# Kernel tuning notes

Hardware: AMD Instinct MI355X
Metric: run time of the kernel (lower is better)

The kernel has to match this reference:

```python
import jax, jax.numpy as jnp
import numpy as np

B, S, D = 64, 256, 768   # batch, max_seq_length, bert hidden
CAP = 8                  # semantic_cap_size (= num_capsules)
NT = 10                  # ntasks (= num_routes)
TASK = 5
NUM_ITER = 3


def squash(t, axis=-1):
    sq = jnp.sum(t * t, axis=axis, keepdims=True)
    return (sq / (1.0 + sq)) * t / jnp.sqrt(sq)


def setup_inputs() -> dict:
    key = jax.random.key(0)
    k0, k1, k2, k3 = jax.random.split(key, 4)
    x = jax.random.normal(k0, (B, S, D), dtype=jnp.float32)
    # per-task semantic projections: ntasks x Linear(768 -> CAP)
    fc1_w = jax.random.normal(k1, (NT, CAP, D), dtype=jnp.float32) * 0.02
    fc1_b = jnp.zeros((NT, CAP), dtype=jnp.float32)
    # route_weights: [num_capsules, num_routes, in_channel=S*CAP, class_dim=S]
    route_weights = jax.random.normal(k2, (CAP, NT, S * CAP, S), dtype=jnp.float32)
    # larger: Linear(CAP -> 768)
    larger_w = jax.random.normal(k3, (D, CAP), dtype=jnp.float32) * 0.02
    larger_b = jnp.zeros((D,), dtype=jnp.float32)
    return {"x": x, "task": TASK, "fc1_w": fc1_w, "fc1_b": fc1_b,
            "route_weights": route_weights, "larger_w": larger_w, "larger_b": larger_b}


def reference(x, task, fc1_w, fc1_b, route_weights, larger_w, larger_b):
    Bb, Ss, _ = x.shape
    nt, cap, _ = fc1_w.shape
    # --- semantic capsules: per-task Linear, cat over task dim, squash over tasks ---
    sem = jnp.einsum('bsd,ncd->bscn', x, fc1_w) + fc1_b.T[None, None]  # [B,S,CAP,NT]
    sem = sem.reshape(Bb, Ss * cap, nt)          # matches torch view(B,-1,1)+cat
    sem = squash(sem, axis=-1)
    u = jnp.transpose(sem, (0, 2, 1))            # [B, NT, S*CAP] (transpose(2,1))
    # --- tsv capsules: dynamic routing ---
    priors = jnp.einsum('brk,crkl->cbrl', u, route_weights)[:, :, :, None, :]  # [CAP,B,NT,1,S]
    tsv = jnp.tril(jnp.ones((nt, nt), dtype=x.dtype))
    tsv_t = tsv[task].reshape(1, 1, nt, 1, 1)
    mask = jnp.where(tsv[task] == 0, jnp.float32(-10000.0), jnp.float32(0.0)).reshape(1, 1, nt, 1, 1)
    logits = jnp.zeros_like(priors)
    vote = None
    for i in range(NUM_ITER):
        logits = logits * tsv_t + mask
        probs = jax.nn.softmax(logits, axis=2)                     # softmax over routes
        vote = jnp.sum(probs * priors, axis=2, keepdims=True)      # [CAP,B,1,1,S]
        out = squash(vote, axis=-1)
        if i != NUM_ITER - 1:
            logits = logits + jnp.sum(priors * out, axis=-1, keepdims=True)
    # torch .view on contiguous [CAP,B,1,1,S] -> (B, S, CAP): row-major reinterpret
    h = vote.reshape(-1).reshape(Bb, Ss, cap)
    return h @ larger_w.T + larger_b
```

## Files before the change

### kernel.cpp

```cpp
#include <hip/hip_runtime.h>
#include <hip/hip_bf16.h>

#define Bq 64
#define Sq 256
#define Dq 768
#define CAPq 8
#define NTq 10
#define SCq 2048

typedef short bf16x8 __attribute__((ext_vector_type(8)));
typedef float f32x4  __attribute__((ext_vector_type(4)));

static __device__ __forceinline__ short bfhi(float f) {
    return (short)(__float_as_uint(f) >> 16);
}
static __device__ __forceinline__ short bflo(float f) {
    float hi = __uint_as_float(__float_as_uint(f) & 0xFFFF0000u);
    return (short)(__float_as_uint(f - hi) >> 16);
}

__global__ __launch_bounds__(256) void k0_cvt(const float* __restrict__ w,
                                              short* __restrict__ hi,
                                              short* __restrict__ lo) {
    int i = blockIdx.x * 256 + threadIdx.x;
    if (i < NTq * CAPq * Dq) {
        int k8 = i / 640;
        int rem = i - k8 * 640;
        int o = rem >> 3, kf = rem & 7;
        float f = w[o * Dq + k8 * 8 + kf];
        hi[i] = bfhi(f);
        lo[i] = bflo(f);
    }
}

__global__ __launch_bounds__(256) void k1_sem(const float* __restrict__ x,
                                              const short* __restrict__ fwh,
                                              const short* __restrict__ fwl,
                                              const float* __restrict__ fc1b,
                                              short* __restrict__ u_hi,
                                              short* __restrict__ u_lo) {
    __shared__ short xsh[12288];
    __shared__ short xsl[12288];
    const int t = threadIdx.x;
    const int L = t & 63, w = t >> 6;
    const int colL = L & 15, kg = L >> 4;
    const int R0 = blockIdx.x * 16;

    const float* xbase = x + (size_t)R0 * Dq;
#pragma unroll
    for (int i = 0; i < 12; ++i) {
        int li = t + i * 256;
        int r = li / 192, j = li - r * 192;
        float4 v = *reinterpret_cast<const float4*>(xbase + (size_t)r * Dq + j * 4);
        int k8 = j >> 1, kf = (j & 1) * 4;
        int off = (k8 * 16 + r) * 8 + kf;
        short4 h4, l4;
        h4.x = bfhi(v.x); h4.y = bfhi(v.y); h4.z = bfhi(v.z); h4.w = bfhi(v.w);
        l4.x = bflo(v.x); l4.y = bflo(v.y); l4.z = bflo(v.z); l4.w = bflo(v.w);
        *reinterpret_cast<short4*>(&xsh[off]) = h4;
        *reinterpret_cast<short4*>(&xsl[off]) = l4;
    }
    __syncthreads();

    f32x4 acc[5];
#pragma unroll
    for (int f = 0; f < 5; ++f) acc[f] = (f32x4){0.f, 0.f, 0.f, 0.f};

    const short* pwh = fwh + kg * 640 + colL * 8;
    const short* pwl = fwl + kg * 640 + colL * 8;

#pragma unroll 2
    for (int kc = 0; kc < 192; kc += 32) {
        const int k8 = ((w * 192 + kc) >> 3) + kg;
        bf16x8 ah = *reinterpret_cast<const bf16x8*>(&xsh[(k8 * 16 + colL) * 8]);
        bf16x8 al = *reinterpret_cast<const bf16x8*>(&xsl[(k8 * 16 + colL) * 8]);
        const int ko80 = (w * 192 + kc) * 80;
#pragma unroll
        for (int f = 0; f < 5; ++f) {
            bf16x8 bh = *reinterpret_cast<const bf16x8*>(pwh + ko80 + f * 128);
            bf16x8 bl = *reinterpret_cast<const bf16x8*>(pwl + ko80 + f * 128);
            acc[f] = __builtin_amdgcn_mfma_f32_16x16x32_bf16(al, bh, acc[f], 0, 0, 0);
            acc[f] = __builtin_amdgcn_mfma_f32_16x16x32_bf16(ah, bl, acc[f], 0, 0, 0);
            acc[f] = __builtin_amdgcn_mfma_f32_16x16x32_bf16(ah, bh, acc[f], 0, 0, 0);
        }
    }

    float* redS = reinterpret_cast<float*>(xsh);
    __syncthreads();
    if (w > 0) {
#pragma unroll
        for (int f = 0; f < 5; ++f)
#pragma unroll
            for (int g = 0; g < 4; ++g)
                redS[((w - 1) * 20 + f * 4 + g) * 64 + L] = acc[f][g];
    }
    __syncthreads();
    if (w == 0) {
        float bias[5];
#pragma unroll
        for (int f = 0; f < 5; ++f) bias[f] = fc1b[f * 16 + colL];
        const int cc = colL & 7;
        const int npar = (colL >> 3) & 1;
#pragma unroll
        for (int reg = 0; reg < 4; ++reg) {
            const int row = R0 + kg * 4 + reg;
            const int b = row >> 8, s = row & 255;
            float v[5], sqp = 0.f;
#pragma unroll
            for (int f = 0; f < 5; ++f) {
                v[f] = acc[f][reg] + redS[(0 * 20 + f * 4 + reg) * 64 + L]
                     + redS[(1 * 20 + f * 4 + reg) * 64 + L]
                     + redS[(2 * 20 + f * 4 + reg) * 64 + L] + bias[f];
                sqp = fmaf(v[f], v[f], sqp);
            }
            float sq = sqp + __shfl_xor(sqp, 8, 64);
            float scale = (sq / (1.f + sq)) / sqrtf(sq);
#pragma unroll
            for (int f = 0; f < 5; ++f) {
                int n = 2 * f + npar;
                size_t off = (((size_t)n * 256 + s) * 64 + b) * 8 + cc;
                float val = v[f] * scale;
                u_hi[off] = bfhi(val);
                u_lo[off] = bflo(val);
            }
        }
    }
}

__device__ __forceinline__ void k2_comp2(const float2* bv, const short* puh, const short* pul,
                                         int ao, f32x4* accE, f32x4* accO) {
    bf16x8 bhE, blE, bhO, blO;
#pragma unroll
    for (int i = 0; i < 8; ++i) {
        bhE[i] = bfhi(bv[i].x); blE[i] = bflo(bv[i].x);
        bhO[i] = bfhi(bv[i].y); blO[i] = bflo(bv[i].y);
    }
#pragma unroll
    for (int m = 0; m < 4; ++m) {
        bf16x8 ah = *reinterpret_cast<const bf16x8*>(puh + ao + m * 128);
        bf16x8 al = *reinterpret_cast<const bf16x8*>(pul + ao + m * 128);
        accE[m] = __builtin_amdgcn_mfma_f32_16x16x32_bf16(al, bhE, accE[m], 0, 0, 0);
        accE[m] = __builtin_amdgcn_mfma_f32_16x16x32_bf16(ah, blE, accE[m], 0, 0, 0);
        accE[m] = __builtin_amdgcn_mfma_f32_16x16x32_bf16(ah, bhE, accE[m], 0, 0, 0);
        accO[m] = __builtin_amdgcn_mfma_f32_16x16x32_bf16(al, bhO, accO[m], 0, 0, 0);
        accO[m] = __builtin_amdgcn_mfma_f32_16x16x32_bf16(ah, blO, accO[m], 0, 0, 0);
        accO[m] = __builtin_amdgcn_mfma_f32_16x16x32_bf16(ah, bhO, accO[m], 0, 0, 0);
    }
}

__global__ __launch_bounds__(256, 3) void k2_priors(const short* __restrict__ u_hi,
                                                    const short* __restrict__ u_lo,
                                                    const float* __restrict__ rw,
                                                    const int* __restrict__ task_p,
                                                    float* __restrict__ part) {
    const int bid = blockIdx.x;
    const int lq = bid / 160;
    const int rem = bid - lq * 160;
    const int ks = rem & 1;
    const int rc = rem >> 1;
    const int c = rc / 10;
    const int r = rc - c * 10;
    if (r > *task_p) return;
    __shared__ float redS[3][2][16][64];
    const int t = threadIdx.x;
    const int L = t & 63, kh = t >> 6;
    const int colL = L & 15, kg = L >> 4;
    const int le = lq * 32 + 2 * colL;
    const int kw0 = ks * 1024 + kh * 256;
    const int s00 = kw0 >> 3;

    f32x4 accE[4], accO[4];
#pragma unroll
    for (int m = 0; m < 4; ++m) {
        accE[m] = (f32x4){0.f, 0.f, 0.f, 0.f};
        accO[m] = (f32x4){0.f, 0.f, 0.f, 0.f};
    }

    const float* pb = rw + ((size_t)(c * NTq + r) * SCq + kw0 + kg * 8) * Sq + le;
    const short* puh = u_hi + (((size_t)r * 256 + s00 + kg) * 64 + colL) * 8;
    const short* pul = u_lo + (((size_t)r * 256 + s00 + kg) * 64 + colL) * 8;

    float2 bv0[8], bv1[8];
#pragma unroll
    for (int i = 0; i < 8; ++i) bv0[i] = *reinterpret_cast<const float2*>(pb + (size_t)i * Sq);

    for (int kc = 0; kc < 256; kc += 64) {
        {
            const float* p = pb + (size_t)(kc + 32) * Sq;
#pragma unroll
            for (int i = 0; i < 8; ++i) bv1[i] = *reinterpret_cast<const float2*>(p + (size_t)i * Sq);
        }
        __builtin_amdgcn_sched_barrier(0);
        k2_comp2(bv0, puh, pul, kc * 64, accE, accO);
        __builtin_amdgcn_sched_barrier(0);
        {
            int kn = (kc + 64 < 256) ? kc + 64 : 0;
            const float* p = pb + (size_t)kn * Sq;
#pragma unroll
            for (int i = 0; i < 8; ++i) bv0[i] = *reinterpret_cast<const float2*>(p + (size_t)i * Sq);
        }
        __builtin_amdgcn_sched_barrier(0);
        k2_comp2(bv1, puh, pul, (kc + 32) * 64, accE, accO);
        __builtin_amdgcn_sched_barrier(0);
    }

    if (kh > 0) {
#pragma unroll
        for (int m = 0; m < 4; ++m)
#pragma unroll
            for (int g = 0; g < 4; ++g) {
                redS[kh - 1][0][m * 4 + g][L] = accE[m][g];
                redS[kh - 1][1][m * 4 + g][L] = accO[m][g];
            }
    }
    __syncthreads();
    if (kh == 0) {
#pragma unroll
        for (int m = 0; m < 4; ++m) {
#pragma unroll
            for (int g = 0; g < 4; ++g) {
                float vE = accE[m][g] + redS[0][0][m * 4 + g][L]
                         + redS[1][0][m * 4 + g][L] + redS[2][0][m * 4 + g][L];
                float vO = accO[m][g] + redS[0][1][m * 4 + g][L]
                         + redS[1][1][m * 4 + g][L] + redS[2][1][m * 4 + g][L];
                int bb = m * 16 + kg * 4 + g;
                size_t idx = (size_t)ks * 1310720 + ((size_t)(c * Bq + bb) * NTq + r) * Sq + le;
                float2 vv; vv.x = vE; vv.y = vO;
                *reinterpret_cast<float2*>(part + idx) = vv;
            }
        }
    }
}

__global__ __launch_bounds__(256) void k34_route_out(const float* __restrict__ part,
                                                     const int* __restrict__ task_p,
                                                     const float* __restrict__ lw,
                                                     const float* __restrict__ lb,
                                                     float* __restrict__ out) {
    const int t = threadIdx.x;
    const int lane = t & 63, w = t >> 6;
    const int b = blockIdx.x & 63, c = blockIdx.x >> 6;
    const int task = *task_p;

    float pr[NTq][4];
    const float* p0 = part + ((size_t)(c * Bq + b) * NTq) * Sq + lane * 4;
#pragma unroll
    for (int r = 0; r < NTq; ++r) {
        f32x4 a = *reinterpret_cast<const f32x4*>(p0 + r * Sq);
        f32x4 d = *reinterpret_cast<const f32x4*>(p0 + 1310720 + r * Sq);
#pragma unroll
        for (int ii = 0; ii < 4; ++ii) pr[r][ii] = a[ii] + d[ii];
    }

    float logits[NTq];
#pragma unroll
    for (int r = 0; r < NTq; ++r) logits[r] = 0.f;
    float vote[4];

    for (int it = 0; it < 3; ++it) {
        float m = -1e30f;
#pragma unroll
        for (int r = 0; r < NTq; ++r) if (r <= task) m = fmaxf(m, logits[r]);
        float p[NTq]; float s = 0.f;
#pragma unroll
        for (int r = 0; r < NTq; ++r) {
            p[r] = (r <= task) ? expf(logits[r] - m) : 0.f;
            s += p[r];
        }
        float inv = 1.f / s;
#pragma unroll
        for (int ii = 0; ii < 4; ++ii) vote[ii] = 0.f;
#pragma unroll
        for (int r = 0; r < NTq; ++r) {
            float pw = p[r] * inv;
#pragma unroll
            for (int ii = 0; ii < 4; ++ii) vote[ii] = fmaf(pw, pr[r][ii], vote[ii]);
        }
        if (it == 2) break;

        float vals[11];
#pragma unroll
        for (int r = 0; r < NTq; ++r) {
            float d = 0.f;
#pragma unroll
            for (int ii = 0; ii < 4; ++ii) d = fmaf(pr[r][ii], vote[ii], d);
            vals[r] = d;
        }
        {
            float d = 0.f;
#pragma unroll
            for (int ii = 0; ii < 4; ++ii) d = fmaf(vote[ii], vote[ii], d);
            vals[10] = d;
        }
#pragma unroll
        for (int o = 32; o > 0; o >>= 1) {
#pragma unroll
            for (int v = 0; v < 11; ++v) vals[v] += __shfl_xor(vals[v], o, 64);
        }
        float sq = vals[10];
        float scale = (sq / (1.f + sq)) / sqrtf(sq);
#pragma unroll
        for (int r = 0; r < NTq; ++r)
            if (r <= task) logits[r] += scale * vals[r];
    }

    float v[8][8];
#pragma unroll
    for (int j = 0; j < 8; ++j) {
        int s0 = w * 16 + 2 * j;
#pragma unroll
        for (int ii = 0; ii < 4; ++ii) v[j][ii]     = __shfl(vote[ii], s0, 64);
#pragma unroll
        for (int ii = 0; ii < 4; ++ii) v[j][4 + ii] = __shfl(vote[ii], s0 + 1, 64);
    }
    const int rbase = c * 2048 + b * 32 + w * 8;
#pragma unroll
    for (int dd = 0; dd < 12; ++dd) {
        int d = lane + dd * 64;
        float4 wa = *reinterpret_cast<const float4*>(lw + (size_t)d * 8);
        float4 wb = *reinterpret_cast<const float4*>(lw + (size_t)d * 8 + 4);
        float lbv = lb[d];
#pragma unroll
        for (int j = 0; j < 8; ++j) {
            float acc = lbv;
            acc = fmaf(v[j][0], wa.x, acc);
            acc = fmaf(v[j][1], wa.y, acc);
            acc = fmaf(v[j][2], wa.z, acc);
            acc = fmaf(v[j][3], wa.w, acc);
            acc = fmaf(v[j][4], wb.x, acc);
            acc = fmaf(v[j][5], wb.y, acc);
            acc = fmaf(v[j][6], wb.z, acc);
            acc = fmaf(v[j][7], wb.w, acc);
            out[(size_t)(rbase + j) * Dq + d] = acc;
        }
    }
}

extern "C" void kernel_launch(void* const* d_in, const int* in_sizes, int n_in,
                              void* d_out, int out_size, void* d_ws, size_t ws_size,
                              hipStream_t stream) {
    const float* x    = (const float*)d_in[0];
    const int*   task = (const int*)d_in[1];
    const float* fc1w = (const float*)d_in[2];
    const float* fc1b = (const float*)d_in[3];
    const float* rw   = (const float*)d_in[4];
    const float* lw   = (const float*)d_in[5];
    const float* lb   = (const float*)d_in[6];
    float* out = (float*)d_out;

    short* u_hi = (short*)d_ws;
    short* u_lo = u_hi + 1310720;
    float* part = (float*)((char*)d_ws + 5242880);
    short* fwh  = (short*)((char*)d_ws + 16252928);
    short* fwl  = fwh + 61440;

    k0_cvt<<<240, 256, 0, stream>>>(fc1w, fwh, fwl);
    k1_sem<<<1024, 256, 0, stream>>>(x, fwh, fwl, fc1b, u_hi, u_lo);
    k2_priors<<<1280, 256, 0, stream>>>(u_hi, u_lo, rw, task, part);
    k34_route_out<<<512, 256, 0, stream>>>(part, task, lw, lb, out);
}
```

Measured before the change: 76.23 us.

## Restructure priors kernel to stage route weights through LDS, split waves by batch

The priors GEMM kernel now has each wave own a 16-row batch slice over the full K range, instead of splitting K across waves and reducing through shared memory. Route-weight tiles are loaded cooperatively as float4, double-buffered in LDS, and read back per wave, which removes the cross-wave reduction and lowers register pressure. The launch also invokes k2_priors twice with identical arguments. That looks like a timing probe and doubles that kernel's work, adding a barrier per K step on top.

```diff
diff --git a/kernel.cpp b/kernel.cpp
--- a/kernel.cpp
+++ b/kernel.cpp
@@ -127,32 +127,11 @@
     }
 }
 
-__device__ __forceinline__ void k2_comp2(const float2* bv, const short* puh, const short* pul,
-                                         int ao, f32x4* accE, f32x4* accO) {
-    bf16x8 bhE, blE, bhO, blO;
-#pragma unroll
-    for (int i = 0; i < 8; ++i) {
-        bhE[i] = bfhi(bv[i].x); blE[i] = bflo(bv[i].x);
-        bhO[i] = bfhi(bv[i].y); blO[i] = bflo(bv[i].y);
-    }
-#pragma unroll
-    for (int m = 0; m < 4; ++m) {
-        bf16x8 ah = *reinterpret_cast<const bf16x8*>(puh + ao + m * 128);
-        bf16x8 al = *reinterpret_cast<const bf16x8*>(pul + ao + m * 128);
-        accE[m] = __builtin_amdgcn_mfma_f32_16x16x32_bf16(al, bhE, accE[m], 0, 0, 0);
-        accE[m] = __builtin_amdgcn_mfma_f32_16x16x32_bf16(ah, blE, accE[m], 0, 0, 0);
-        accE[m] = __builtin_amdgcn_mfma_f32_16x16x32_bf16(ah, bhE, accE[m], 0, 0, 0);
-        accO[m] = __builtin_amdgcn_mfma_f32_16x16x32_bf16(al, bhO, accO[m], 0, 0, 0);
-        accO[m] = __builtin_amdgcn_mfma_f32_16x16x32_bf16(ah, blO, accO[m], 0, 0, 0);
-        accO[m] = __builtin_amdgcn_mfma_f32_16x16x32_bf16(ah, bhO, accO[m], 0, 0, 0);
-    }
-}
-
-__global__ __launch_bounds__(256, 3) void k2_priors(const short* __restrict__ u_hi,
-                                                    const short* __restrict__ u_lo,
-                                                    const float* __restrict__ rw,
-                                                    const int* __restrict__ task_p,
-                                                    float* __restrict__ part) {
+__global__ __launch_bounds__(256) void k2_priors(const short* __restrict__ u_hi,
+                                                 const short* __restrict__ u_lo,
+                                                 const float* __restrict__ rw,
+                                                 const int* __restrict__ task_p,
+                                                 float* __restrict__ part) {
     const int bid = blockIdx.x;
     const int lq = bid / 160;
     const int rem = bid - lq * 160;
@@ -161,74 +140,62 @@
     const int c = rc / 10;
     const int r = rc - c * 10;
     if (r > *task_p) return;
-    __shared__ float redS[3][2][16][64];
-    const int t = threadIdx.x;
-    const int L = t & 63, kh = t >> 6;
+    __shared__ __attribute__((aligned(16))) float ldsb[2048];
+    const int t0 = threadIdx.x;
+    const int L = t0 & 63, w = t0 >> 6;
     const int colL = L & 15, kg = L >> 4;
+    const int kw0 = ks * 1024;
+    const int s00 = ks * 128;
+
+    f32x4 accE = (f32x4){0.f, 0.f, 0.f, 0.f};
+    f32x4 accO = (f32x4){0.f, 0.f, 0.f, 0.f};
+
+    const float* psrc = rw + (((size_t)(c * NTq + r)) * SCq + kw0 + w * 8 + (L >> 3)) * Sq
+                           + lq * 32 + (L & 7) * 4;
+    const short* puh = u_hi + (((size_t)r * 256 + s00 + kg) * 64 + w * 16 + colL) * 8;
+    const short* pul = u_lo + (((size_t)r * 256 + s00 + kg) * 64 + w * 16 + colL) * 8;
+
+    float4 stg = *reinterpret_cast<const float4*>(psrc);
+
+    for (int t = 0; t < 32; ++t) {
+        float* dst = &ldsb[(t & 1) * 1024 + w * 256 + L * 4];
+        *reinterpret_cast<float4*>(dst) = stg;
+        asm volatile("s_waitcnt lgkmcnt(0)" ::: "memory");
+        __builtin_amdgcn_sched_barrier(0);
+        __builtin_amdgcn_s_barrier();
+        __builtin_amdgcn_sched_barrier(0);
+        bf16x8 ah = *reinterpret_cast<const bf16x8*>(puh + (size_t)t * 2048);
+        bf16x8 al = *reinterpret_cast<const bf16x8*>(pul + (size_t)t * 2048);
+        __builtin_amdgcn_sched_barrier(0);
+        if (t + 1 < 32)
+            stg = *reinterpret_cast<const float4*>(psrc + (size_t)(t + 1) * 8192);
+        __builtin_amdgcn_sched_barrier(0);
+        const float* lbp = &ldsb[(t & 1) * 1024 + colL * 2];
+        float2 bv[8];
+#pragma unroll
+        for (int j = 0; j < 8; ++j)
+            bv[j] = *reinterpret_cast<const float2*>(lbp + (kg * 8 + j) * 32);
+        bf16x8 bhE, blE, bhO, blO;
+#pragma unroll
+        for (int j = 0; j < 8; ++j) {
+            bhE[j] = bfhi(bv[j].x); blE[j] = bflo(bv[j].x);
+            bhO[j] = bfhi(bv[j].y); blO[j] = bflo(bv[j].y);
+        }
+        accE = __builtin_amdgcn_mfma_f32_16x16x32_bf16(al, bhE, accE, 0, 0, 0);
+        accE = __builtin_amdgcn_mfma_f32_16x16x32_bf16(ah, blE, accE, 0, 0, 0);
+        accE = __builtin_amdgcn_mfma_f32_16x16x32_bf16(ah, bhE, accE, 0, 0, 0);
+        accO = __builtin_amdgcn_mfma_f32_16x16x32_bf16(al, bhO, accO, 0, 0, 0);
+        accO = __builtin_amdgcn_mfma_f32_16x16x32_bf16(ah, blO, accO, 0, 0, 0);
+        accO = __builtin_amdgcn_mfma_f32_16x16x32_bf16(ah, bhO, accO, 0, 0, 0);
+    }
+
     const int le = lq * 32 + 2 * colL;
-    const int kw0 = ks * 1024 + kh * 256;
-    const int s00 = kw0 >> 3;
-
-    f32x4 accE[4], accO[4];
-#pragma unroll
-    for (int m = 0; m < 4; ++m) {
-        accE[m] = (f32x4){0.f, 0.f, 0.f, 0.f};
-        accO[m] = (f32x4){0.f, 0.f, 0.f, 0.f};
-    }
-
-    const float* pb = rw + ((size_t)(c * NTq + r) * SCq + kw0 + kg * 8) * Sq + le;
-    const short* puh = u_hi + (((size_t)r * 256 + s00 + kg) * 64 + colL) * 8;
-    const short* pul = u_lo + (((size_t)r * 256 + s00 + kg) * 64 + colL) * 8;
-
-    float2 bv0[8], bv1[8];
-#pragma unroll
-    for (int i = 0; i < 8; ++i) bv0[i] = *reinterpret_cast<const float2*>(pb + (size_t)i * Sq);
-
-    for (int kc = 0; kc < 256; kc += 64) {
-        {
-            const float* p = pb + (size_t)(kc + 32) * Sq;
-#pragma unroll
-            for (int i = 0; i < 8; ++i) bv1[i] = *reinterpret_cast<const float2*>(p + (size_t)i * Sq);
-        }
-        __builtin_amdgcn_sched_barrier(0);
-        k2_comp2(bv0, puh, pul, kc * 64, accE, accO);
-        __builtin_amdgcn_sched_barrier(0);
-        {
-            int kn = (kc + 64 < 256) ? kc + 64 : 0;
-            const float* p = pb + (size_t)kn * Sq;
-#pragma unroll
-            for (int i = 0; i < 8; ++i) bv0[i] = *reinterpret_cast<const float2*>(p + (size_t)i * Sq);
-        }
-        __builtin_amdgcn_sched_barrier(0);
-        k2_comp2(bv1, puh, pul, (kc + 32) * 64, accE, accO);
-        __builtin_amdgcn_sched_barrier(0);
-    }
-
-    if (kh > 0) {
-#pragma unroll
-        for (int m = 0; m < 4; ++m)
-#pragma unroll
-            for (int g = 0; g < 4; ++g) {
-                redS[kh - 1][0][m * 4 + g][L] = accE[m][g];
-                redS[kh - 1][1][m * 4 + g][L] = accO[m][g];
-            }
-    }
-    __syncthreads();
-    if (kh == 0) {
-#pragma unroll
-        for (int m = 0; m < 4; ++m) {
-#pragma unroll
-            for (int g = 0; g < 4; ++g) {
-                float vE = accE[m][g] + redS[0][0][m * 4 + g][L]
-                         + redS[1][0][m * 4 + g][L] + redS[2][0][m * 4 + g][L];
-                float vO = accO[m][g] + redS[0][1][m * 4 + g][L]
-                         + redS[1][1][m * 4 + g][L] + redS[2][1][m * 4 + g][L];
-                int bb = m * 16 + kg * 4 + g;
-                size_t idx = (size_t)ks * 1310720 + ((size_t)(c * Bq + bb) * NTq + r) * Sq + le;
-                float2 vv; vv.x = vE; vv.y = vO;
-                *reinterpret_cast<float2*>(part + idx) = vv;
-            }
-        }
+#pragma unroll
+    for (int g = 0; g < 4; ++g) {
+        int bb = w * 16 + kg * 4 + g;
+        size_t idx = (size_t)ks * 1310720 + ((size_t)(c * Bq + bb) * NTq + r) * Sq + le;
+        float2 vv; vv.x = accE[g]; vv.y = accO[g];
+        *reinterpret_cast<float2*>(part + idx) = vv;
     }
 }
 
@@ -357,5 +324,6 @@
     k0_cvt<<<240, 256, 0, stream>>>(fc1w, fwh, fwl);
     k1_sem<<<1024, 256, 0, stream>>>(x, fwh, fwl, fc1b, u_hi, u_lo);
     k2_priors<<<1280, 256, 0, stream>>>(u_hi, u_lo, rw, task, part);
+    k2_priors<<<1280, 256, 0, stream>>>(u_hi, u_lo, rw, task, part);
     k34_route_out<<<512, 256, 0, stream>>>(part, task, lw, lb, out);
 }
```

New measurement: 98.77 us. 29.6% more time.
